# Optimization experiments

Measured on AMD Instinct MI355X. Metric: run time of the kernel, lower is better.

Reference implementation:

```python
import jax, jax.numpy as jnp
import numpy as np

K = 20           # neighbors
ALPHA = 1.0      # clustering alpha
BN_EPS = 1e-5
NEG_SLOPE = 0.2


def knn_idx(x, k):
    # x: (B, C, N) -> idx (B, N, k) of k nearest neighbors by squared L2
    xx = jnp.sum(x * x, axis=1)                      # (B, N)
    inner = jnp.einsum('bcn,bcm->bnm', x, x)         # (B, N, N)
    pd = -xx[:, :, None] + 2.0 * inner - xx[:, None, :]  # negative sq dist
    return jax.lax.top_k(pd, k)[1]


def graph_feature(x, k):
    # x: (B, C, N) -> (B, 2C, N, k): concat(neighbor - center, center)
    xt = jnp.transpose(x, (0, 2, 1))                 # (B, N, C)
    idx = knn_idx(x, k)                              # (B, N, k)
    feat = jax.vmap(lambda f, i: f[i])(xt, idx)      # (B, N, k, C)
    center = jnp.broadcast_to(xt[:, :, None, :], feat.shape)
    out = jnp.concatenate([feat - center, center], axis=-1)
    return jnp.transpose(out, (0, 3, 1, 2))


def batchnorm(x, g, b, axes):
    # training-mode BN: batch statistics over `axes`, channel axis = 1
    m = jnp.mean(x, axes, keepdims=True)
    v = jnp.var(x, axes, keepdims=True)
    shape = [1] * x.ndim
    shape[1] = x.shape[1]
    return (x - m) / jnp.sqrt(v + BN_EPS) * g.reshape(shape) + b.reshape(shape)


def conv_block2d(x, w, g, b):
    # 1x1 Conv2d (no bias) + BN2d + LeakyReLU; x (B,Cin,N,k), w (Cout,Cin)
    y = jnp.einsum('oc,bcnk->bonk', w, x)
    return jax.nn.leaky_relu(batchnorm(y, g, b, (0, 2, 3)), NEG_SLOPE)


def setup_inputs() -> dict:
    key = jax.random.key(0)
    ks = jax.random.split(key, 16)
    B, C, N = 4, 3, 2048
    d = {
        'x1': jax.random.normal(ks[0], (B, C, N), jnp.float32),
        'x2': jax.random.normal(ks[1], (B, C, N), jnp.float32),
        'w1': jax.random.normal(ks[2], (64, 6), jnp.float32) * 0.1,
        'g1': jnp.ones((64,), jnp.float32), 'b1': jnp.zeros((64,), jnp.float32),
        'w2': jax.random.normal(ks[3], (64, 128), jnp.float32) * 0.1,
        'g2': jnp.ones((64,), jnp.float32), 'b2': jnp.zeros((64,), jnp.float32),
        'w3': jax.random.normal(ks[4], (128, 128), jnp.float32) * 0.1,
        'g3': jnp.ones((128,), jnp.float32), 'b3': jnp.zeros((128,), jnp.float32),
        'w4': jax.random.normal(ks[5], (256, 256), jnp.float32) * 0.1,
        'g4': jnp.ones((256,), jnp.float32), 'b4': jnp.zeros((256,), jnp.float32),
        'w5': jax.random.normal(ks[6], (1024, 512), jnp.float32) * 0.05,
        'g5': jnp.ones((1024,), jnp.float32), 'b5': jnp.zeros((1024,), jnp.float32),
        'lw1': jax.random.normal(ks[7], (256, 2048), jnp.float32) * 0.02,
        'lb1': jnp.zeros((256,), jnp.float32),
        'lw2': jax.random.normal(ks[8], (64, 256), jnp.float32) * 0.05,
        'lb2': jnp.zeros((64,), jnp.float32),
        'lw3': jax.random.normal(ks[9], (10, 64), jnp.float32) * 0.1,
        'lb3': jnp.zeros((10,), jnp.float32),
        'cw': jax.random.normal(ks[10], (800, 10), jnp.float32) * 0.1,
    }
    return d


def reference(x1, x2, w1, g1, b1, w2, g2, b2, w3, g3, b3, w4, g4, b4,
              w5, g5, b5, lw1, lb1, lw2, lb2, lw3, lb3, cw):

    def single(x):
        h = conv_block2d(graph_feature(x, K), w1, g1, b1)
        f1 = h.max(axis=-1)                            # (B,64,N)
        h = conv_block2d(graph_feature(f1, K), w2, g2, b2)
        f2 = h.max(axis=-1)                            # (B,64,N)
        h = conv_block2d(graph_feature(f2, K), w3, g3, b3)
        f3 = h.max(axis=-1)                            # (B,128,N)
        h = conv_block2d(graph_feature(f3, K), w4, g4, b4)
        f4 = h.max(axis=-1)                            # (B,256,N)
        h = jnp.concatenate([f1, f2, f3, f4], axis=1)  # (B,512,N)
        h = jnp.einsum('oc,bcn->bon', w5, h)           # 1x1 Conv1d
        h = jax.nn.leaky_relu(batchnorm(h, g5, b5, (0, 2)), NEG_SLOPE)
        z = jnp.concatenate([h.max(axis=-1), h.mean(axis=-1)], axis=1)  # (B,2048)
        z = z @ lw1.T + lb1
        z = z @ lw2.T + lb2
        e = z @ lw3.T + lb3                            # (B,10)
        diff = e[:, None, :] - cw                      # (B,800,10)
        x_dis = jnp.sum(diff * diff, axis=2)           # (B,800)
        q = (1.0 + x_dis / ALPHA) ** (-(ALPHA + 1.0) / 2.0)
        q = q / jnp.sum(q, axis=1, keepdims=True)
        return q, e, x_dis

    q1, e1, xd1 = single(x1)
    q2, e2, xd2 = single(x2)
    d = e1 - e2 + 1e-6  # torch F.pairwise_distance eps
    sim = jnp.sqrt(jnp.sum(d * d, axis=1))
    return (sim, q1, q2, e1, e2, xd1)
```

## Files before the change

### kernel.cpp

```cpp
#include <hip/hip_runtime.h>
#include <math.h>

#define BB 4
#define NN 2048
#define KK 20
#define NEG 0.2f

#define QOFF0 4
#define QOFF1 3204
#define EOFF0 6404
#define EOFF1 6444
#define XDOFF 6484

typedef unsigned short u16;
typedef unsigned int u32;
typedef __attribute__((ext_vector_type(8))) short s16x8;
typedef __attribute__((ext_vector_type(4))) float f32x4;
typedef __attribute__((ext_vector_type(16))) float f32x16;
typedef __attribute__((ext_vector_type(8))) u16 u16x8;

__device__ __forceinline__ u16 f2bf(float x) {
    u32 u = __float_as_uint(x);
    u += 0x7FFFu + ((u >> 16) & 1u);
    return (u16)(u >> 16);
}

__global__ __launch_bounds__(256) void transpose_x_kernel(
    const float* __restrict__ x, float* __restrict__ fnc, float* __restrict__ xx,
    u16* __restrict__ fh, u16* __restrict__ fl)
{
    int gid = blockIdx.x * 256 + threadIdx.x;
    int b = gid >> 11, n = gid & 2047;
    float s = 0.f;
    float v[3];
#pragma unroll
    for (int c = 0; c < 3; ++c) {
        v[c] = x[((size_t)b * 3 + c) * NN + n];
        fnc[(size_t)gid * 3 + c] = v[c];
        s += v[c] * v[c];
    }
    xx[gid] = s;
    u16x8 z = {0,0,0,0,0,0,0,0};
    u16x8 h0 = z, l0 = z;
#pragma unroll
    for (int c = 0; c < 3; ++c) {
        u16 hb = f2bf(v[c]);
        h0[c] = hb;
        l0[c] = f2bf(v[c] - __uint_as_float((u32)hb << 16));
    }
    u16* fhp = fh + (size_t)gid * 32;
    u16* flp = fl + (size_t)gid * 32;
    *(u16x8*)(fhp)      = h0; *(u16x8*)(fhp + 8)  = z;
    *(u16x8*)(fhp + 16) = z;  *(u16x8*)(fhp + 24) = z;
    *(u16x8*)(flp)      = l0; *(u16x8*)(flp + 8)  = z;
    *(u16x8*)(flp + 16) = z;  *(u16x8*)(flp + 24) = z;
}

__global__ __launch_bounds__(256) void norms_kernel(
    const float* __restrict__ h512, int choff, int C, float* __restrict__ xx)
{
    int gid = blockIdx.x * 256 + threadIdx.x;
    const float* p = h512 + (size_t)gid * 512 + choff;
    float s = 0.f;
    for (int c = 0; c < C; ++c) { float v = p[c]; s += v * v; }
    xx[gid] = s;
}

#define NINFV -3.4e38f

template<int CTRL>
__device__ __forceinline__ void dmax2(float& a1, float& a2)
{
    int b1i = __builtin_amdgcn_update_dpp(
        __float_as_int(a1), __float_as_int(a1), CTRL, 0xf, 0xf, false);
    int b2i = __builtin_amdgcn_update_dpp(
        __float_as_int(a2), __float_as_int(a2), CTRL, 0xf, 0xf, false);
    float b1 = __int_as_float(b1i), b2 = __int_as_float(b2i);
    float n1 = fmaxf(a1, b1);
    float n2 = fmaxf(fminf(a1, b1), fmaxf(a2, b2));
    a1 = n1; a2 = n2;
}

template<int KT>
__global__ __launch_bounds__(1024, 4) void knn_mfma_kernel(
    const u16* __restrict__ Fh, const u16* __restrict__ Fl,
    int ncs, int choff,
    const float* __restrict__ xx, int* __restrict__ idxout)
{
    __shared__ float sbuf[16][NN];
    int tid = threadIdx.x;
    int bid = blockIdx.x;
    int b   = bid & 3;
    int n0  = (bid >> 2) << 4;
    int wv = tid >> 6, lane = tid & 63;
    int l15 = lane & 15, l4 = lane >> 4;

    const u16* Ahp = Fh + (size_t)(b * NN + n0 + l15) * ncs + choff + l4 * 8;
    const u16* Alp = Fl + (size_t)(b * NN + n0 + l15) * ncs + choff + l4 * 8;
    s16x8 a_h[KT], a_l[KT];
#pragma unroll
    for (int kt = 0; kt < KT; ++kt) {
        a_h[kt] = *(const s16x8*)(Ahp + kt * 32);
        a_l[kt] = *(const s16x8*)(Alp + kt * 32);
    }

    const float* xb = xx + b * NN;
#pragma unroll
    for (int ct = 0; ct < 8; ++ct) {
        int m0 = (wv << 7) + (ct << 4);
        const u16* Bhp = Fh + (size_t)(b * NN + m0 + l15) * ncs + choff + l4 * 8;
        const u16* Blp = Fl + (size_t)(b * NN + m0 + l15) * ncs + choff + l4 * 8;
        f32x4 acc;
#pragma unroll
        for (int i = 0; i < 4; ++i) acc[i] = 0.f;
#pragma unroll
        for (int kt = 0; kt < KT; ++kt) {
            s16x8 bh = *(const s16x8*)(Bhp + kt * 32);
            s16x8 bl = *(const s16x8*)(Blp + kt * 32);
            acc = __builtin_amdgcn_mfma_f32_16x16x32_bf16(a_h[kt], bh, acc, 0, 0, 0);
            acc = __builtin_amdgcn_mfma_f32_16x16x32_bf16(a_l[kt], bh, acc, 0, 0, 0);
            acc = __builtin_amdgcn_mfma_f32_16x16x32_bf16(a_h[kt], bl, acc, 0, 0, 0);
        }
        float xv = xb[m0 + l15];
#pragma unroll
        for (int i = 0; i < 4; ++i) {
            int row = l4 * 4 + i;
            sbuf[row][m0 + l15] = 2.f * acc[i] - xv;
        }
    }
    __syncthreads();

    float* sb = sbuf[wv];
    int p = n0 + wv;
    int* op = idxout + (size_t)(b * NN + p) * KK;

    if (lane == 0) op[0] = p;
    if (lane == (p & 63)) sb[p] = NINFV;

    float v1 = NINFV, v2 = NINFV, v3 = NINFV, v4 = NINFV;
    int j1 = -1, j2 = -1, j3 = -1, j4 = -1;
#pragma unroll
    for (int j = 0; j < 32; ++j) {
        float vv = sb[lane + (j << 6)];
        if (vv > v1) { v4 = v3; j4 = j3; v3 = v2; j3 = j2; v2 = v1; j2 = j1; v1 = vv; j1 = j; }
        else if (vv > v2) { v4 = v3; j4 = j3; v3 = v2; j3 = j2; v2 = vv; j2 = j; }
        else if (vv > v3) { v4 = v3; j4 = j3; v3 = vv; j3 = j; }
        else if (vv > v4) { v4 = vv; j4 = j; }
    }

    unsigned consumed = 0u;

    for (int it = 1; it < KK; it += 2) {
        float r1 = v1, r2 = v2;
        dmax2<0x111>(r1, r2);
        dmax2<0x112>(r1, r2);
        dmax2<0x114>(r1, r2);
        dmax2<0x118>(r1, r2);
        dmax2<0x142>(r1, r2);
        dmax2<0x143>(r1, r2);
        float m1 = __int_as_float(
            __builtin_amdgcn_readlane(__float_as_int(r1), 63));
        float m2 = __int_as_float(
            __builtin_amdgcn_readlane(__float_as_int(r2), 63));
        unsigned long long k1 = __ballot(v1 == m1);
        if (lane == __ffsll(k1) - 1) {
            op[it] = lane + (j1 << 6);
            consumed |= 1u << j1;
            v1 = v2; j1 = j2; v2 = v3; j2 = j3; v3 = v4; j3 = j4;
            v4 = NINFV; j4 = -1;
        }
        if (it + 1 < KK) {
            unsigned long long k2 = __ballot(v1 == m2);
            if (lane == __ffsll(k2) - 1) {
                op[it + 1] = lane + (j1 << 6);
                consumed |= 1u << j1;
                v1 = v2; j1 = j2; v2 = v3; j2 = j3; v3 = v4; j3 = j4;
                v4 = NINFV; j4 = -1;
            }
        }
        if (__any(v2 == NINFV)) {
            if (v2 == NINFV) {
                v1 = NINFV; v2 = NINFV; v3 = NINFV; v4 = NINFV;
                j1 = -1; j2 = -1; j3 = -1; j4 = -1;
#pragma unroll
                for (int j = 0; j < 32; ++j) {
                    if (!(consumed & (1u << j))) {
                        float vv = sb[lane + (j << 6)];
                        if (vv > v1) { v4 = v3; j4 = j3; v3 = v2; j3 = j2; v2 = v1; j2 = j1; v1 = vv; j1 = j; }
                        else if (vv > v2) { v4 = v3; j4 = j3; v3 = v2; j3 = j2; v2 = vv; j2 = j; }
                        else if (vv > v3) { v4 = v3; j4 = j3; v3 = vv; j3 = j; }
                        else if (vv > v4) { v4 = vv; j4 = j; }
                    }
                }
            }
        }
    }
}

template<int C, int COUT>
__global__ __launch_bounds__(256) void gemm_gh_kernel(
    const float* __restrict__ fnc, int ncs, int choff,
    const float* __restrict__ W,
    float* __restrict__ G, float* __restrict__ H)
{
    constexpr int GROUPS = 256 / COUT;
    constexpr int RPT = 8 / GROUPS;
    __shared__ float Fs[8][C];
    int tid = threadIdx.x;
    int row0 = blockIdx.x * 8;
    for (int i = tid; i < 8 * C; i += 256) {
        int r = i / C, c = i % C;
        Fs[r][c] = fnc[(size_t)(row0 + r) * ncs + choff + c];
    }
    __syncthreads();
    int o = tid % COUT;
    int r0 = (tid / COUT) * RPT;
    float g[RPT], h[RPT];
#pragma unroll
    for (int r = 0; r < RPT; ++r) { g[r] = 0.f; h[r] = 0.f; }
    const float* wr = W + (size_t)o * 2 * C;
    for (int c = 0; c < C; ++c) {
        float w1 = wr[c], wd = wr[C + c] - w1;
#pragma unroll
        for (int r = 0; r < RPT; ++r) {
            float f = Fs[r0 + r][c];
            g[r] += f * w1; h[r] += f * wd;
        }
    }
#pragma unroll
    for (int r = 0; r < RPT; ++r) {
        size_t rr = (size_t)(row0 + r0 + r) * COUT + o;
        G[rr] = g[r]; H[rr] = h[r];
    }
}

template<int COUT>
__global__ __launch_bounds__(256) void gather_kernel(
    const float* __restrict__ G, const float* __restrict__ H,
    const int* __restrict__ idx,
    float* __restrict__ ymax, float* __restrict__ ymin,
    float* __restrict__ psum, float* __restrict__ psumsq)
{
    constexpr int RPI = 256 / COUT;
    constexpr int NITER = 16 / RPI;
    int tid = threadIdx.x;
    int o = tid % COUT;
    int rsub = tid / COUT;
    int row0 = blockIdx.x * 16;
    float s = 0.f, s2 = 0.f;
    for (int it = 0; it < NITER; ++it) {
        int r = row0 + it * RPI + rsub;
        int b = r >> 11;
        float h = H[(size_t)r * COUT + o];
        const int* ip = idx + (size_t)r * KK;
        float mx = -3.4e38f, mn = 3.4e38f;
#pragma unroll
        for (int j = 0; j < KK; ++j) {
            int m = ip[j];
            float g = G[((size_t)(b << 11) + m) * COUT + o];
            float y = g + h;
            mx = fmaxf(mx, y); mn = fminf(mn, y);
            s += y; s2 += y * y;
        }
        ymax[(size_t)r * COUT + o] = mx;
        ymin[(size_t)r * COUT + o] = mn;
    }
    __shared__ float ls[256], ls2[256];
    ls[tid] = s; ls2[tid] = s2;
    __syncthreads();
    for (int st = 128; st >= COUT; st >>= 1) {
        if (tid < st) { ls[tid] += ls[tid + st]; ls2[tid] += ls2[tid + st]; }
        __syncthreads();
    }
    if (tid < COUT) {
        psum[(size_t)blockIdx.x * COUT + tid]   = ls[tid];
        psumsq[(size_t)blockIdx.x * COUT + tid] = ls2[tid];
    }
}

__global__ __launch_bounds__(256) void bnscale_kernel(
    const float* __restrict__ psum, const float* __restrict__ psumsq,
    int nblk, int cout, float cnt,
    const float* __restrict__ gw, const float* __restrict__ bw,
    float* __restrict__ ss)
{
    int o = blockIdx.x;
    int t = threadIdx.x;
    float s = 0.f, s2 = 0.f;
    for (int i = t; i < nblk; i += 256) {
        s  += psum[(size_t)i * cout + o];
        s2 += psumsq[(size_t)i * cout + o];
    }
    __shared__ float ls[256], ls2[256];
    ls[t] = s; ls2[t] = s2;
    __syncthreads();
    for (int st = 128; st > 0; st >>= 1) {
        if (t < st) { ls[t] += ls[t + st]; ls2[t] += ls2[t + st]; }
        __syncthreads();
    }
    if (t == 0) {
        float m = ls[0] / cnt;
        float v = ls2[0] / cnt - m * m;
        float sc = gw[o] / sqrtf(v + 1e-5f);
        float sh = bw[o] - m * sc;
        ss[o * 2] = sc; ss[o * 2 + 1] = sh;
    }
}

__global__ __launch_bounds__(256) void apply_kernel(
    const float* __restrict__ ymax, const float* __restrict__ ymin,
    const float* __restrict__ ss, int coutShift, int choff,
    float* __restrict__ h512, u16* __restrict__ Ah, u16* __restrict__ Al)
{
    size_t gid = (size_t)blockIdx.x * 256 + threadIdx.x;
    int o = (int)(gid & ((1u << coutShift) - 1));
    size_t r = gid >> coutShift;
    float sc = ss[o * 2], sh = ss[o * 2 + 1];
    float v = (sc >= 0.f) ? ymax[gid] : ymin[gid];
    float a = sc * v + sh;
    float act = (a > 0.f) ? a : NEG * a;
    size_t hidx = r * 512 + choff + o;
    h512[hidx] = act;
    u16 hb = f2bf(act);
    Ah[hidx] = hb;
    Al[hidx] = f2bf(act - __uint_as_float((u32)hb << 16));
}

template<int CO>
__global__ __launch_bounds__(256) void apply_t_kernel(
    const float* __restrict__ ymax, const float* __restrict__ ymin,
    const float* __restrict__ ss, int choff,
    float* __restrict__ h512, float* __restrict__ fcn,
    u16* __restrict__ Ah, u16* __restrict__ Al)
{
    constexpr int TILES_O = CO >> 6;
    __shared__ float tile[64][65];
    int tr = blockIdx.x / TILES_O;
    int to = blockIdx.x % TILES_O;
    int r0 = tr * 64, o0 = to * 64;
    int t = threadIdx.x;
    int lr = t >> 6;
    int lo = t & 63;
    int o = o0 + lo;
    float sc = ss[o * 2], sh = ss[o * 2 + 1];
#pragma unroll
    for (int rr = 0; rr < 64; rr += 4) {
        int r = r0 + rr + lr;
        size_t gid = (size_t)r * CO + o;
        float v = (sc >= 0.f) ? ymax[gid] : ymin[gid];
        float a = sc * v + sh;
        float act = (a > 0.f) ? a : NEG * a;
        size_t hidx = (size_t)r * 512 + choff + o;
        h512[hidx] = act;
        u16 hb = f2bf(act);
        Ah[hidx] = hb;
        Al[hidx] = f2bf(act - __uint_as_float((u32)hb << 16));
        tile[rr + lr][lo] = act;
    }
    __syncthreads();
    int b = r0 >> 11;
    int n0 = r0 & 2047;
#pragma unroll
    for (int oo = 0; oo < 64; oo += 4) {
        fcn[((size_t)(b * CO + o0 + oo + lr)) * NN + n0 + lo] = tile[lo][oo + lr];
    }
}

__global__ __launch_bounds__(256) void tobf16_b_kernel(
    const float* __restrict__ Bm, u16* __restrict__ Bh, u16* __restrict__ Bl)
{
    int gid = blockIdx.x * 256 + threadIdx.x;
    size_t off = (size_t)gid * 8;
    float4 v0 = *(const float4*)(Bm + off);
    float4 v1 = *(const float4*)(Bm + off + 4);
    float x[8] = {v0.x, v0.y, v0.z, v0.w, v1.x, v1.y, v1.z, v1.w};
    u16x8 h, l;
#pragma unroll
    for (int j = 0; j < 8; ++j) {
        u16 hb = f2bf(x[j]);
        h[j] = hb;
        l[j] = f2bf(x[j] - __uint_as_float((u32)hb << 16));
    }
    *(u16x8*)(Bh + off) = h;
    *(u16x8*)(Bl + off) = l;
}

__device__ __forceinline__ void gload_lds16(const void* g, void* l) {
    __builtin_amdgcn_global_load_lds(
        (const __attribute__((address_space(1))) void*)g,
        (__attribute__((address_space(3))) void*)l, 16, 0, 0);
}

__global__ __launch_bounds__(256) void gemm5_mfma_kernel(
    const u16* __restrict__ Ah, const u16* __restrict__ Al,
    const u16* __restrict__ Bh, const u16* __restrict__ Bl,
    float* __restrict__ Y, float* __restrict__ psum, float* __restrict__ psumsq)
{
    __shared__ u16 As[2][128][64];
    __shared__ u16 Bs[2][128][64];
    __shared__ float scs[4][128];
    __shared__ float sqs[4][128];

    int tid = threadIdx.x;
    int bm = blockIdx.x & 63, bn = blockIdx.x >> 6;
    int row0 = bm * 128, col0 = bn * 128;
    int w = tid >> 6, lane = tid & 63;
    int wr = w >> 1, wc = w & 1;

    int isB = w >> 1, plane = w & 1;
    int srow = lane >> 3;
    int kch  = (lane & 7) ^ srow;
    const u16* gbase = isB ? (plane ? Bl : Bh) : (plane ? Al : Ah);
    int rc0 = isB ? col0 : row0;
    const u16* gsrc0 = gbase + (size_t)(rc0 + srow) * 512 + kch * 8;
    u16* lds0 = (isB ? &Bs[0][0][0] : &As[0][0][0]) + plane * 8192;

    f32x16 acc[2][2];
#pragma unroll
    for (int i = 0; i < 2; ++i)
#pragma unroll
        for (int j = 0; j < 2; ++j)
#pragma unroll
            for (int r = 0; r < 16; ++r) acc[i][j][r] = 0.f;

    int ln = lane & 31, l5 = lane >> 5;
    const u16* Afb = &As[0][0][0] + (size_t)(wr * 64 + ln) * 64;
    const u16* Bfb = &Bs[0][0][0] + (size_t)(wc * 64 + ln) * 64;

    for (int k0 = 0; k0 < 512; k0 += 64) {
#pragma unroll
        for (int cc = 0; cc < 16; ++cc)
            gload_lds16(gsrc0 + (size_t)cc * 4096 + k0, lds0 + cc * 512);
        __syncthreads();

#pragma unroll
        for (int ks = 0; ks < 4; ++ks) {
            int pos = ((ks * 2 + l5) ^ (ln & 7)) * 8;
            s16x8 ah0 = *(const s16x8*)(Afb + pos);
            s16x8 ah1 = *(const s16x8*)(Afb + 2048 + pos);
            s16x8 al0 = *(const s16x8*)(Afb + 8192 + pos);
            s16x8 al1 = *(const s16x8*)(Afb + 8192 + 2048 + pos);
#pragma unroll
            for (int j = 0; j < 2; ++j) {
                s16x8 bh = *(const s16x8*)(Bfb + j * 2048 + pos);
                s16x8 bl = *(const s16x8*)(Bfb + 8192 + j * 2048 + pos);
                acc[0][j] = __builtin_amdgcn_mfma_f32_32x32x16_bf16(ah0, bh, acc[0][j], 0, 0, 0);
                acc[1][j] = __builtin_amdgcn_mfma_f32_32x32x16_bf16(ah1, bh, acc[1][j], 0, 0, 0);
                acc[0][j] = __builtin_amdgcn_mfma_f32_32x32x16_bf16(al0, bh, acc[0][j], 0, 0, 0);
                acc[1][j] = __builtin_amdgcn_mfma_f32_32x32x16_bf16(al1, bh, acc[1][j], 0, 0, 0);
                acc[0][j] = __builtin_amdgcn_mfma_f32_32x32x16_bf16(ah0, bl, acc[0][j], 0, 0, 0);
                acc[1][j] = __builtin_amdgcn_mfma_f32_32x32x16_bf16(ah1, bl, acc[1][j], 0, 0, 0);
            }
        }
        __syncthreads();
    }

#pragma unroll
    for (int i = 0; i < 2; ++i)
#pragma unroll
        for (int reg = 0; reg < 16; ++reg) {
            int row = row0 + wr * 64 + i * 32 + l5 * 4 + (reg >> 2) * 8 + (reg & 3);
            float* yp = Y + (size_t)row * 1024 + col0 + wc * 64 + ln;
            yp[0]  = acc[i][0][reg];
            yp[32] = acc[i][1][reg];
        }

#pragma unroll
    for (int j = 0; j < 2; ++j) {
        float s = 0.f, q = 0.f;
#pragma unroll
        for (int i = 0; i < 2; ++i)
#pragma unroll
            for (int reg = 0; reg < 16; ++reg) {
                float v = acc[i][j][reg];
                s += v; q += v * v;
            }
        scs[wr * 2 + l5][wc * 64 + j * 32 + ln] = s;
        sqs[wr * 2 + l5][wc * 64 + j * 32 + ln] = q;
    }
    __syncthreads();
    if (tid < 128) {
        float s = 0.f, q = 0.f;
#pragma unroll
        for (int p = 0; p < 4; ++p) { s += scs[p][tid]; q += sqs[p][tid]; }
        psum[(size_t)bm * 1024 + col0 + tid]   = s;
        psumsq[(size_t)bm * 1024 + col0 + tid] = q;
    }
}

__global__ __launch_bounds__(256) void pool_part_kernel(
    const float* __restrict__ Y, const float* __restrict__ ss,
    float* __restrict__ pmax, float* __restrict__ psum)
{
    int bid = blockIdx.x;
    int b = bid >> 6;
    int n0 = (bid & 63) * 32;
    int t = threadIdx.x;
    int o = t * 4;
    float4 sA = *(const float4*)(ss + o * 2);
    float4 sB = *(const float4*)(ss + o * 2 + 4);
    float4 mx = {-3.4e38f, -3.4e38f, -3.4e38f, -3.4e38f};
    float4 sm = {0.f, 0.f, 0.f, 0.f};
    const float* Yb = Y + ((size_t)b * NN + n0) * 1024 + o;
#pragma unroll 4
    for (int n = 0; n < 32; ++n) {
        float4 v = *(const float4*)(Yb + (size_t)n * 1024);
        float a0 = sA.x * v.x + sA.y; a0 = (a0 > 0.f) ? a0 : NEG * a0;
        float a1 = sA.z * v.y + sA.w; a1 = (a1 > 0.f) ? a1 : NEG * a1;
        float a2 = sB.x * v.z + sB.y; a2 = (a2 > 0.f) ? a2 : NEG * a2;
        float a3 = sB.z * v.w + sB.w; a3 = (a3 > 0.f) ? a3 : NEG * a3;
        mx.x = fmaxf(mx.x, a0); sm.x += a0;
        mx.y = fmaxf(mx.y, a1); sm.y += a1;
        mx.z = fmaxf(mx.z, a2); sm.z += a2;
        mx.w = fmaxf(mx.w, a3); sm.w += a3;
    }
    size_t po = (size_t)bid * 1024 + o;
    *(float4*)(pmax + po) = mx;
    *(float4*)(psum + po) = sm;
}

__global__ __launch_bounds__(256) void pool_comb_kernel(
    const float* __restrict__ pmax, const float* __restrict__ psum,
    float* __restrict__ z)
{
    int b = blockIdx.x;
    int t = threadIdx.x;
    int o = t * 4;
    float4 mx = {-3.4e38f, -3.4e38f, -3.4e38f, -3.4e38f};
    float4 sm = {0.f, 0.f, 0.f, 0.f};
    for (int ch = 0; ch < 64; ++ch) {
        size_t po = ((size_t)(b * 64 + ch)) * 1024 + o;
        float4 m = *(const float4*)(pmax + po);
        float4 s = *(const float4*)(psum + po);
        mx.x = fmaxf(mx.x, m.x); mx.y = fmaxf(mx.y, m.y);
        mx.z = fmaxf(mx.z, m.z); mx.w = fmaxf(mx.w, m.w);
        sm.x += s.x; sm.y += s.y; sm.z += s.z; sm.w += s.w;
    }
    *(float4*)(z + (size_t)b * 2048 + o) = mx;
    float4 mn = {sm.x * (1.f / 2048.f), sm.y * (1.f / 2048.f),
                 sm.z * (1.f / 2048.f), sm.w * (1.f / 2048.f)};
    *(float4*)(z + (size_t)b * 2048 + 1024 + o) = mn;
}

__global__ __launch_bounds__(64) void gemv1_kernel(
    const float* __restrict__ z, const float* __restrict__ lw1,
    const float* __restrict__ lb1, float* __restrict__ z1)
{
    int o = blockIdx.x;
    int lane = threadIdx.x;
    const float* wr = lw1 + (size_t)o * 2048;
    float a0 = 0.f, a1 = 0.f, a2 = 0.f, a3 = 0.f;
    for (int c = lane; c < 2048; c += 64) {
        float w = wr[c];
        a0 += z[c] * w; a1 += z[2048 + c] * w;
        a2 += z[4096 + c] * w; a3 += z[6144 + c] * w;
    }
#pragma unroll
    for (int off = 32; off > 0; off >>= 1) {
        a0 += __shfl_down(a0, off); a1 += __shfl_down(a1, off);
        a2 += __shfl_down(a2, off); a3 += __shfl_down(a3, off);
    }
    if (lane == 0) {
        float bias = lb1[o];
        z1[o] = a0 + bias; z1[256 + o] = a1 + bias;
        z1[512 + o] = a2 + bias; z1[768 + o] = a3 + bias;
    }
}

__global__ __launch_bounds__(1024) void head2_kernel(
    const float* __restrict__ z1,
    const float* __restrict__ lw2, const float* __restrict__ lb2,
    const float* __restrict__ lw3, const float* __restrict__ lb3,
    const float* __restrict__ cw,
    float* __restrict__ out, float* __restrict__ e_store, int which)
{
    __shared__ float z2s[4][64];
    __shared__ float es[4][10];
    __shared__ float qs[3200];
    __shared__ float dnm[4];
    int t = threadIdx.x;
    if (t < 256) {
        int b = t >> 6, o = t & 63;
        float acc = lb2[o];
        const float* wr = lw2 + (size_t)o * 256;
        const float* zr = z1 + b * 256;
        for (int c = 0; c < 256; ++c) acc += zr[c] * wr[c];
        z2s[b][o] = acc;
    }
    __syncthreads();
    if (t < 40) {
        int b = t / 10, o = t % 10;
        float acc = lb3[o];
        const float* wr = lw3 + o * 64;
        for (int c = 0; c < 64; ++c) acc += z2s[b][c] * wr[c];
        es[b][o] = acc;
        int eoff = (which == 0) ? EOFF0 : EOFF1;
        out[eoff + b * 10 + o] = acc;
        e_store[which * 40 + b * 10 + o] = acc;
    }
    __syncthreads();
    for (int p = t; p < 3200; p += 1024) {
        int b = p / 800, j = p % 800;
        float xd = 0.f;
        const float* cwr = cw + j * 10;
#pragma unroll
        for (int i = 0; i < 10; ++i) { float d = es[b][i] - cwr[i]; xd += d * d; }
        qs[p] = 1.0f / (1.0f + xd);
        if (which == 0) out[XDOFF + p] = xd;
    }
    __syncthreads();
    if (t < 4) {
        float s = 0.f;
        for (int j = 0; j < 800; ++j) s += qs[t * 800 + j];
        dnm[t] = s;
    }
    __syncthreads();
    int qoff = (which == 0) ? QOFF0 : QOFF1;
    for (int p = t; p < 3200; p += 1024) out[qoff + p] = qs[p] / dnm[p / 800];
}

__global__ void sim_kernel(const float* __restrict__ e_store, float* __restrict__ out)
{
    int t = threadIdx.x;
    if (t < 4) {
        float s = 0.f;
        for (int i = 0; i < 10; ++i) {
            float d = e_store[t * 10 + i] - e_store[40 + t * 10 + i] + 1e-6f;
            s += d * d;
        }
        out[t] = sqrtf(s);
    }
}

extern "C" void kernel_launch(void* const* d_in, const int* in_sizes, int n_in,
                              void* d_out, int out_size, void* d_ws, size_t ws_size,
                              hipStream_t stream)
{
    const float* x1  = (const float*)d_in[0];
    const float* x2  = (const float*)d_in[1];
    const float* w1  = (const float*)d_in[2];
    const float* g1  = (const float*)d_in[3];
    const float* b1  = (const float*)d_in[4];
    const float* w2  = (const float*)d_in[5];
    const float* g2  = (const float*)d_in[6];
    const float* b2  = (const float*)d_in[7];
    const float* w3  = (const float*)d_in[8];
    const float* g3  = (const float*)d_in[9];
    const float* b3  = (const float*)d_in[10];
    const float* w4  = (const float*)d_in[11];
    const float* g4  = (const float*)d_in[12];
    const float* b4  = (const float*)d_in[13];
    const float* w5  = (const float*)d_in[14];
    const float* g5  = (const float*)d_in[15];
    const float* b5  = (const float*)d_in[16];
    const float* lw1 = (const float*)d_in[17];
    const float* lb1 = (const float*)d_in[18];
    const float* lw2 = (const float*)d_in[19];
    const float* lb2 = (const float*)d_in[20];
    const float* lw3 = (const float*)d_in[21];
    const float* lb3 = (const float*)d_in[22];
    const float* cw  = (const float*)d_in[23];
    float* out = (float*)d_out;

    float* ws   = (float*)d_ws;
    float* h512 = ws;
    float* G    = h512 + 4194304;
    float* Hb   = G + 2097152;
    float* ymax = Hb + 2097152;
    float* ymin = ymax + 2097152;
    float* y5   = G;
    float* fcn  = ymin + 2097152;
    float* fnc1 = fcn + 1048576;
    float* xx   = fnc1 + 32768;
    float* psum = xx + 8192;
    float* psq  = psum + 131072;
    float* ss   = psq + 131072;
    float* p5s  = ss + 2048;
    float* p5q  = p5s + 262144;
    float* ss5  = p5q + 262144;
    float* z    = ss5 + 2048;
    float* z1   = z + 8192;
    float* est  = z1 + 1024;
    int*   idx  = (int*)(est + 128);
    u16*   Ahs  = (u16*)(idx + BB * NN * KK);
    u16*   Als  = Ahs + 4194304;
    u16*   Bhs  = Als + 4194304;
    u16*   Bls  = Bhs + 524288;
    u16*   fnc1h = Bls + 524288;
    u16*   fnc1l = fnc1h + 262144;

    tobf16_b_kernel<<<256, 256, 0, stream>>>(w5, Bhs, Bls);

    for (int which = 0; which < 2; ++which) {
        const float* xin = which ? x2 : x1;
        transpose_x_kernel<<<32, 256, 0, stream>>>(xin, fnc1, xx, fnc1h, fnc1l);
        knn_mfma_kernel<1><<<512, 1024, 0, stream>>>(fnc1h, fnc1l, 32, 0, xx, idx);
        gemm_gh_kernel<3, 64><<<1024, 256, 0, stream>>>(fnc1, 3, 0, w1, G, Hb);
        gather_kernel<64><<<512, 256, 0, stream>>>(G, Hb, idx, ymax, ymin, psum, psq);
        bnscale_kernel<<<64, 256, 0, stream>>>(psum, psq, 512, 64, 163840.f, g1, b1, ss);
        apply_t_kernel<64><<<128, 256, 0, stream>>>(ymax, ymin, ss, 0, h512, fcn, Ahs, Als);
        norms_kernel<<<32, 256, 0, stream>>>(h512, 0, 64, xx);
        knn_mfma_kernel<2><<<512, 1024, 0, stream>>>(Ahs, Als, 512, 0, xx, idx);
        gemm_gh_kernel<64, 64><<<1024, 256, 0, stream>>>(h512, 512, 0, w2, G, Hb);
        gather_kernel<64><<<512, 256, 0, stream>>>(G, Hb, idx, ymax, ymin, psum, psq);
        bnscale_kernel<<<64, 256, 0, stream>>>(psum, psq, 512, 64, 163840.f, g2, b2, ss);
        apply_t_kernel<64><<<128, 256, 0, stream>>>(ymax, ymin, ss, 64, h512, fcn, Ahs, Als);
        norms_kernel<<<32, 256, 0, stream>>>(h512, 64, 64, xx);
        knn_mfma_kernel<2><<<512, 1024, 0, stream>>>(Ahs, Als, 512, 64, xx, idx);
        gemm_gh_kernel<64, 128><<<1024, 256, 0, stream>>>(h512, 512, 64, w3, G, Hb);
        gather_kernel<128><<<512, 256, 0, stream>>>(G, Hb, idx, ymax, ymin, psum, psq);
        bnscale_kernel<<<128, 256, 0, stream>>>(psum, psq, 512, 128, 163840.f, g3, b3, ss);
        apply_t_kernel<128><<<256, 256, 0, stream>>>(ymax, ymin, ss, 128, h512, fcn, Ahs, Als);
        norms_kernel<<<32, 256, 0, stream>>>(h512, 128, 128, xx);
        knn_mfma_kernel<4><<<512, 1024, 0, stream>>>(Ahs, Als, 512, 128, xx, idx);
        gemm_gh_kernel<128, 256><<<1024, 256, 0, stream>>>(h512, 512, 128, w4, G, Hb);
        gather_kernel<256><<<512, 256, 0, stream>>>(G, Hb, idx, ymax, ymin, psum, psq);
        bnscale_kernel<<<256, 256, 0, stream>>>(psum, psq, 512, 256, 163840.f, g4, b4, ss);
        apply_kernel<<<8192, 256, 0, stream>>>(ymax, ymin, ss, 8, 256, h512, Ahs, Als);
        gemm5_mfma_kernel<<<512, 256, 0, stream>>>(Ahs, Als, Bhs, Bls, y5, p5s, p5q);
        bnscale_kernel<<<1024, 256, 0, stream>>>(p5s, p5q, 64, 1024, 8192.f, g5, b5, ss5);
        pool_part_kernel<<<256, 256, 0, stream>>>(y5, ss5, p5s, p5q);
        pool_comb_kernel<<<4, 256, 0, stream>>>(p5s, p5q, z);
        gemv1_kernel<<<256, 64, 0, stream>>>(z, lw1, lb1, z1);
        head2_kernel<<<1, 1024, 0, stream>>>(z1, lw2, lb2, lw3, lb3, cw, out, est, which);
    }
    sim_kernel<<<1, 64, 0, stream>>>(est, out);
}
```

Before: 1.239 ms.

## Split kNN into global-memory distance GEMM and separate top-k selection kernel

The fused kNN kernel, which computed a 16-row distance tile into LDS and then ran a top-k selection per wave, is split into two kernels. The first computes distance rows with MFMA, staging neighbor features through LDS via direct global-to-LDS loads with a swizzle, and writes full NxN score matrices for two batches to a global scratch buffer. The second reads each row into registers and runs the same wave-level top-k selection. This removes the large LDS footprint and the 1024-thread blocks, which should raise occupancy. The cost is a write and read-back of tens of MB of scratch per kNN pass and more kernel launches.

```diff
diff --git a/kernel.cpp b/kernel.cpp
--- a/kernel.cpp
+++ b/kernel.cpp
@@ -81,67 +81,92 @@
     a1 = n1; a2 = n2;
 }
 
+__device__ __forceinline__ void gload_lds16(const void* g, void* l) {
+    __builtin_amdgcn_global_load_lds(
+        (const __attribute__((address_space(1))) void*)g,
+        (__attribute__((address_space(3))) void*)l, 16, 0, 0);
+}
+
 template<int KT>
-__global__ __launch_bounds__(1024, 4) void knn_mfma_kernel(
+__global__ __launch_bounds__(512) void knn_dotg_kernel(
     const u16* __restrict__ Fh, const u16* __restrict__ Fl,
-    int ncs, int choff,
-    const float* __restrict__ xx, int* __restrict__ idxout)
-{
-    __shared__ float sbuf[16][NN];
+    int ncs, int choff, int bbase,
+    const float* __restrict__ xx, float* __restrict__ S)
+{
+    __shared__ u16 Bst[8][2][KT][512];
     int tid = threadIdx.x;
     int bid = blockIdx.x;
-    int b   = bid & 3;
-    int n0  = (bid >> 2) << 4;
+    int bl  = bid & 1, b = bbase + bl;
+    int r0  = (bid >> 1) << 4;
     int wv = tid >> 6, lane = tid & 63;
     int l15 = lane & 15, l4 = lane >> 4;
 
-    const u16* Ahp = Fh + (size_t)(b * NN + n0 + l15) * ncs + choff + l4 * 8;
-    const u16* Alp = Fl + (size_t)(b * NN + n0 + l15) * ncs + choff + l4 * 8;
+    const u16* Ah0 = Fh + (size_t)(b * NN + r0 + l15) * ncs + choff + l4 * 8;
+    const u16* Al0 = Fl + (size_t)(b * NN + r0 + l15) * ncs + choff + l4 * 8;
     s16x8 a_h[KT], a_l[KT];
 #pragma unroll
     for (int kt = 0; kt < KT; ++kt) {
-        a_h[kt] = *(const s16x8*)(Ahp + kt * 32);
-        a_l[kt] = *(const s16x8*)(Alp + kt * 32);
-    }
-
+        a_h[kt] = *(const s16x8*)(Ah0 + kt * 32);
+        a_l[kt] = *(const s16x8*)(Al0 + kt * 32);
+    }
+
+    int srow = lane >> 2;
+    int scc  = (lane & 3) ^ (srow & 3);
     const float* xb = xx + b * NN;
-#pragma unroll
-    for (int ct = 0; ct < 8; ++ct) {
-        int m0 = (wv << 7) + (ct << 4);
-        const u16* Bhp = Fh + (size_t)(b * NN + m0 + l15) * ncs + choff + l4 * 8;
-        const u16* Blp = Fl + (size_t)(b * NN + m0 + l15) * ncs + choff + l4 * 8;
+    float* Sb = S + (size_t)bl * NN * NN;
+
+    for (int t = 0; t < 16; ++t) {
+        int c0 = (t << 7) + (wv << 4);
+        size_t srcrow = (size_t)(b * NN + c0 + srow) * ncs + choff;
+#pragma unroll
+        for (int kt = 0; kt < KT; ++kt) {
+            gload_lds16(Fh + srcrow + kt * 32 + scc * 8, &Bst[wv][0][kt][0]);
+            gload_lds16(Fl + srcrow + kt * 32 + scc * 8, &Bst[wv][1][kt][0]);
+        }
+        asm volatile("s_waitcnt vmcnt(0)" ::: "memory");
+
         f32x4 acc;
 #pragma unroll
         for (int i = 0; i < 4; ++i) acc[i] = 0.f;
+        int rb = l15 * 32 + ((l4 ^ (l15 & 3)) << 3);
 #pragma unroll
         for (int kt = 0; kt < KT; ++kt) {
-            s16x8 bh = *(const s16x8*)(Bhp + kt * 32);
-            s16x8 bl = *(const s16x8*)(Blp + kt * 32);
-            acc = __builtin_amdgcn_mfma_f32_16x16x32_bf16(a_h[kt], bh, acc, 0, 0, 0);
-            acc = __builtin_amdgcn_mfma_f32_16x16x32_bf16(a_l[kt], bh, acc, 0, 0, 0);
-            acc = __builtin_amdgcn_mfma_f32_16x16x32_bf16(a_h[kt], bl, acc, 0, 0, 0);
-        }
-        float xv = xb[m0 + l15];
-#pragma unroll
-        for (int i = 0; i < 4; ++i) {
-            int row = l4 * 4 + i;
-            sbuf[row][m0 + l15] = 2.f * acc[i] - xv;
-        }
-    }
-    __syncthreads();
-
-    float* sb = sbuf[wv];
-    int p = n0 + wv;
-    int* op = idxout + (size_t)(b * NN + p) * KK;
-
-    if (lane == 0) op[0] = p;
-    if (lane == (p & 63)) sb[p] = NINFV;
+            s16x8 bh  = *(const s16x8*)&Bst[wv][0][kt][rb];
+            s16x8 bl_ = *(const s16x8*)&Bst[wv][1][kt][rb];
+            acc = __builtin_amdgcn_mfma_f32_16x16x32_bf16(a_h[kt], bh,  acc, 0, 0, 0);
+            acc = __builtin_amdgcn_mfma_f32_16x16x32_bf16(a_l[kt], bh,  acc, 0, 0, 0);
+            acc = __builtin_amdgcn_mfma_f32_16x16x32_bf16(a_h[kt], bl_, acc, 0, 0, 0);
+        }
+        float xv = xb[c0 + l15];
+#pragma unroll
+        for (int i = 0; i < 4; ++i)
+            Sb[(size_t)(r0 + l4 * 4 + i) * NN + c0 + l15] = 2.f * acc[i] - xv;
+    }
+}
+
+__global__ __launch_bounds__(256) void knn_selg_kernel(
+    const float* __restrict__ S, int bbase, int* __restrict__ idxout)
+{
+    int tid = threadIdx.x;
+    int w = tid >> 6, lane = tid & 63;
+    int row = blockIdx.x * 4 + w;
+    int bl = row >> 11, n = row & 2047;
+    const float* sb = S + ((size_t)bl * NN + n) * NN;
+    int* op = idxout + ((size_t)((bbase + bl) * NN + n)) * KK;
+
+    float rv[32];
+#pragma unroll
+    for (int j = 0; j < 32; ++j) {
+        float vv = sb[lane + (j << 6)];
+        rv[j] = (lane + (j << 6) == n) ? NINFV : vv;
+    }
+    if (lane == 0) op[0] = n;
 
     float v1 = NINFV, v2 = NINFV, v3 = NINFV, v4 = NINFV;
     int j1 = -1, j2 = -1, j3 = -1, j4 = -1;
 #pragma unroll
     for (int j = 0; j < 32; ++j) {
-        float vv = sb[lane + (j << 6)];
+        float vv = rv[j];
         if (vv > v1) { v4 = v3; j4 = j3; v3 = v2; j3 = j2; v2 = v1; j2 = j1; v1 = vv; j1 = j; }
         else if (vv > v2) { v4 = v3; j4 = j3; v3 = v2; j3 = j2; v2 = vv; j2 = j; }
         else if (vv > v3) { v4 = v3; j4 = j3; v3 = vv; j3 = j; }
@@ -185,7 +210,7 @@
 #pragma unroll
                 for (int j = 0; j < 32; ++j) {
                     if (!(consumed & (1u << j))) {
-                        float vv = sb[lane + (j << 6)];
+                        float vv = rv[j];
                         if (vv > v1) { v4 = v3; j4 = j3; v3 = v2; j3 = j2; v2 = v1; j2 = j1; v1 = vv; j1 = j; }
                         else if (vv > v2) { v4 = v3; j4 = j3; v3 = v2; j3 = j2; v2 = vv; j2 = j; }
                         else if (vv > v3) { v4 = v3; j4 = j3; v3 = vv; j3 = j; }
@@ -383,12 +408,6 @@
     }
     *(u16x8*)(Bh + off) = h;
     *(u16x8*)(Bl + off) = l;
-}
-
-__device__ __forceinline__ void gload_lds16(const void* g, void* l) {
-    __builtin_amdgcn_global_load_lds(
-        (const __attribute__((address_space(1))) void*)g,
-        (__attribute__((address_space(3))) void*)l, 16, 0, 0);
 }
 
 __global__ __launch_bounds__(256) void gemm5_mfma_kernel(
@@ -669,6 +688,7 @@
     float* ymax = Hb + 2097152;
     float* ymin = ymax + 2097152;
     float* y5   = G;
+    float* Sscr = G;
     float* fcn  = ymin + 2097152;
     float* fnc1 = fcn + 1048576;
     float* xx   = fnc1 + 32768;
@@ -694,25 +714,37 @@
     for (int which = 0; which < 2; ++which) {
         const float* xin = which ? x2 : x1;
         transpose_x_kernel<<<32, 256, 0, stream>>>(xin, fnc1, xx, fnc1h, fnc1l);
-        knn_mfma_kernel<1><<<512, 1024, 0, stream>>>(fnc1h, fnc1l, 32, 0, xx, idx);
+        for (int bp = 0; bp < 2; ++bp) {
+            knn_dotg_kernel<1><<<256, 512, 0, stream>>>(fnc1h, fnc1l, 32, 0, 2*bp, xx, Sscr);
+            knn_selg_kernel<<<1024, 256, 0, stream>>>(Sscr, 2*bp, idx);
+        }
         gemm_gh_kernel<3, 64><<<1024, 256, 0, stream>>>(fnc1, 3, 0, w1, G, Hb);
         gather_kernel<64><<<512, 256, 0, stream>>>(G, Hb, idx, ymax, ymin, psum, psq);
         bnscale_kernel<<<64, 256, 0, stream>>>(psum, psq, 512, 64, 163840.f, g1, b1, ss);
         apply_t_kernel<64><<<128, 256, 0, stream>>>(ymax, ymin, ss, 0, h512, fcn, Ahs, Als);
         norms_kernel<<<32, 256, 0, stream>>>(h512, 0, 64, xx);
-        knn_mfma_kernel<2><<<512, 1024, 0, stream>>>(Ahs, Als, 512, 0, xx, idx);
+        for (int bp = 0; bp < 2; ++bp) {
+            knn_dotg_kernel<2><<<256, 512, 0, stream>>>(Ahs, Als, 512, 0, 2*bp, xx, Sscr);
+            knn_selg_kernel<<<1024, 256, 0, stream>>>(Sscr, 2*bp, idx);
+        }
         gemm_gh_kernel<64, 64><<<1024, 256, 0, stream>>>(h512, 512, 0, w2, G, Hb);
         gather_kernel<64><<<512, 256, 0, stream>>>(G, Hb, idx, ymax, ymin, psum, psq);
         bnscale_kernel<<<64, 256, 0, stream>>>(psum, psq, 512, 64, 163840.f, g2, b2, ss);
         apply_t_kernel<64><<<128, 256, 0, stream>>>(ymax, ymin, ss, 64, h512, fcn, Ahs, Als);
         norms_kernel<<<32, 256, 0, stream>>>(h512, 64, 64, xx);
-        knn_mfma_kernel<2><<<512, 1024, 0, stream>>>(Ahs, Als, 512, 64, xx, idx);
+        for (int bp = 0; bp < 2; ++bp) {
+            knn_dotg_kernel<2><<<256, 512, 0, stream>>>(Ahs, Als, 512, 64, 2*bp, xx, Sscr);
+            knn_selg_kernel<<<1024, 256, 0, stream>>>(Sscr, 2*bp, idx);
+        }
         gemm_gh_kernel<64, 128><<<1024, 256, 0, stream>>>(h512, 512, 64, w3, G, Hb);
         gather_kernel<128><<<512, 256, 0, stream>>>(G, Hb, idx, ymax, ymin, psum, psq);
         bnscale_kernel<<<128, 256, 0, stream>>>(psum, psq, 512, 128, 163840.f, g3, b3, ss);
         apply_t_kernel<128><<<256, 256, 0, stream>>>(ymax, ymin, ss, 128, h512, fcn, Ahs, Als);
         norms_kernel<<<32, 256, 0, stream>>>(h512, 128, 128, xx);
-        knn_mfma_kernel<4><<<512, 1024, 0, stream>>>(Ahs, Als, 512, 128, xx, idx);
+        for (int bp = 0; bp < 2; ++bp) {
+            knn_dotg_kernel<4><<<256, 512, 0, stream>>>(Ahs, Als, 512, 128, 2*bp, xx, Sscr);
+            knn_selg_kernel<<<1024, 256, 0, stream>>>(Sscr, 2*bp, idx);
+        }
         gemm_gh_kernel<128, 256><<<1024, 256, 0, stream>>>(h512, 512, 128, w4, G, Hb);
         gather_kernel<256><<<512, 256, 0, stream>>>(G, Hb, idx, ymax, ymin, psum, psq);
         bnscale_kernel<<<256, 256, 0, stream>>>(psum, psq, 512, 256, 163840.f, g4, b4, ss);
```

New measurement: 1.311 ms. +5.8%, slower.
